# Kernel tuning notes

Measured on AMD Instinct MI355X. Metric: run time of the kernel, lower is better.

## Reference

```python
import jax, jax.numpy as jnp
import numpy as np


def _update_cv(features, labels, ave, cov, amount, class_num):
    # Segment-reduce formulation of the onehot-expand update_CV.
    N, A = features.shape
    C = class_num
    counts = jax.ops.segment_sum(jnp.ones((N,), features.dtype), labels, num_segments=C)  # [C]
    sums = jax.ops.segment_sum(features, labels, num_segments=C)  # [C, A]
    denom = jnp.where(counts == 0, 1.0, counts)[:, None]  # Amount_CxA with zeros -> 1
    ave_CxA = sums / denom
    # var_temp: sum over samples of (x - mean_label)^2, divided by count
    diff = features - ave_CxA[labels]  # [N, A]
    sq = jax.ops.segment_sum(diff * diff, labels, num_segments=C)
    var_temp = sq / denom
    sum_weight = counts[:, None]  # [C,1] broadcast over A
    weight_CV = sum_weight / (sum_weight + amount[:, None])
    weight_CV = jnp.nan_to_num(weight_CV, nan=0.0)
    additional_CV = weight_CV * (1 - weight_CV) * (ave - ave_CxA) ** 2
    new_cov = cov * (1 - weight_CV) + var_temp * weight_CV + additional_CV
    new_ave = ave * (1 - weight_CV) + ave_CxA * weight_CV
    new_amount = amount + counts
    return new_ave, new_cov, new_amount


def _isda_aug(fc_weight, y, labels, cv_matrix, ratio):
    # sigma2[n,c] = ratio * sum_a (W[c,a] - W[labels[n],a])^2 * CV[labels[n],a]
    # = ratio * ( (W^2) @ cv_n - 2 W @ (w_n * cv_n) + sum_a w_n^2 cv_n )
    cv_n = cv_matrix[labels]              # [N, A]
    w_n = fc_weight[labels]               # [N, A]
    t1 = cv_n @ (fc_weight ** 2).T        # [N, C]
    t2 = (w_n * cv_n) @ fc_weight.T       # [N, C]
    t3 = jnp.sum(w_n * w_n * cv_n, axis=1, keepdims=True)  # [N, 1]
    sigma2 = ratio * (t1 - 2.0 * t2 + t3)
    return y + 0.5 * sigma2


def setup_inputs() -> dict:
    key = jax.random.key(0)
    k1, k2, k3, k4 = jax.random.split(key, 4)
    N, A, C = 512, 2048, 1000
    features = jax.random.normal(k1, (N, A), dtype=jnp.float32)
    labels = jax.random.randint(k2, (N,), 0, C)
    fc_weight = jax.random.normal(k3, (C, A), dtype=jnp.float32) * 0.02
    fc_bias = jax.random.normal(k4, (C,), dtype=jnp.float32) * 0.02
    return {
        "features": features,
        "labels": labels,
        "fc_weight": fc_weight,
        "fc_bias": fc_bias,
        "ave_state": jnp.zeros((C, A), jnp.float32),
        "cov_state": jnp.zeros((C, A), jnp.float32),
        "amount_state": jnp.zeros((C,), jnp.float32),
        "ratio": 1,
    }


def reference(features, labels, fc_weight, fc_bias, ave_state, cov_state, amount_state, ratio):
    C = fc_weight.shape[0]
    # model head: y = features @ W^T + b (features come from backbone; detached for CV)
    y = features @ fc_weight.T + fc_bias
    new_ave, new_cov, new_amount = _update_cv(
        jax.lax.stop_gradient(features), labels, ave_state, cov_state, amount_state, C)
    isda_y = _isda_aug(fc_weight, y, labels, jax.lax.stop_gradient(new_cov), ratio)
    log_probs = jax.nn.log_softmax(isda_y, axis=1)
    loss = -jnp.mean(jnp.take_along_axis(log_probs, labels[:, None], axis=1))
    return loss, y, new_ave, new_cov, new_amount
```

## Files before the change

kernel.cpp:

```cpp
#include <hip/hip_runtime.h>
#include <hip/hip_bf16.h>

typedef short v8s __attribute__((ext_vector_type(8)));
typedef float v4f __attribute__((ext_vector_type(4)));

#define KSPLIT 4

static __device__ __forceinline__ float ldv(const void* p, size_t i, int f32m) {
    if (f32m) return ((const float*)p)[i];
    return __bfloat162float(((const __hip_bfloat16*)p)[i]);
}
static __device__ __forceinline__ void stv(void* p, size_t i, float v, int f32m) {
    if (f32m) ((float*)p)[i] = v;
    else ((__hip_bfloat16*)p)[i] = __float2bfloat16(v);
}
static __device__ __forceinline__ unsigned short f2bu(float x) {
    __hip_bfloat16 h = __float2bfloat16(x);
    return *(unsigned short*)&h;
}

static __device__ __forceinline__ float decode_scalar(const void* p) {
    unsigned u = *(const unsigned*)p;
    unsigned e32 = (u >> 23) & 0xff;
    if (e32 >= 97 && e32 <= 160) return __uint_as_float(u);
    unsigned lo = u & 0xffffu;
    unsigned e16 = (lo >> 7) & 0xff;
    if ((u >> 16) == 0 && e16 >= 97 && e16 <= 160)
        return __uint_as_float(lo << 16);
    return (float)(int)u;
}

static __device__ __forceinline__ int block_sniff(const void* feat) {
    const __hip_bfloat16* p = (const __hip_bfloat16*)feat;
    float v = __bfloat162float(p[threadIdx.x & 255]);
    int bad = !(fabsf(v) < 1e10f);
    return __syncthreads_or(bad) ? 1 : 0;
}

__device__ __forceinline__ float wave_sum(float v) {
    #pragma unroll
    for (int o = 32; o > 0; o >>= 1) v += __shfl_down(v, o, 64);
    return v;
}
__device__ __forceinline__ float wave_max(float v) {
    #pragma unroll
    for (int o = 32; o > 0; o >>= 1) v = fmaxf(v, __shfl_down(v, o, 64));
    return v;
}

static __device__ __forceinline__ void ld16(unsigned short* lds, const unsigned short* g) {
    __builtin_amdgcn_global_load_lds(
        (const __attribute__((address_space(1))) unsigned int*)g,
        (__attribute__((address_space(3))) unsigned int*)lds,
        16, 0, 0);
}

__global__ __launch_bounds__(256) void accum_stats(
        const void* __restrict__ feat, const int* __restrict__ labels,
        float* __restrict__ sums, float* __restrict__ sqs,
        float* __restrict__ counts, unsigned short* __restrict__ featb,
        int Nn, int A) {
    int f32m = block_sniff(feat);
    int idx = blockIdx.x * 256 + threadIdx.x;
    if (idx >= Nn * A) return;
    int n = idx / A;
    int a = idx - n * A;
    int l = labels[n];
    float x = ldv(feat, idx, f32m);
    featb[idx] = f2bu(x);
    atomicAdd(&sums[(size_t)l * A + a], x);
    atomicAdd(&sqs[(size_t)l * A + a], x * x);
    if (a == 0) atomicAdd(&counts[l], 1.0f);
}

__global__ __launch_bounds__(256) void finalize_stats(
        const float* __restrict__ sums, const float* __restrict__ sqs,
        const float* __restrict__ counts,
        const void* __restrict__ ave, const void* __restrict__ cov,
        const void* __restrict__ amount, const void* __restrict__ W,
        const void* __restrict__ feat,
        void* __restrict__ out, size_t off_ave, size_t off_cov, size_t off_amt,
        unsigned short* __restrict__ Wb, unsigned short* __restrict__ W2b,
        unsigned short* __restrict__ Cb, unsigned short* __restrict__ Gb,
        float* __restrict__ T3c,
        int C, int A) {
    __shared__ float sb[4];
    int f32m = block_sniff(feat);
    int idx = blockIdx.x * 256 + threadIdx.x;
    int c = idx / A;
    int a = idx - c * A;
    float cnt = counts[c];
    float denom = cnt > 0.f ? cnt : 1.f;
    float mean = sums[idx] / denom;
    float var = (sqs[idx] - cnt * mean * mean) / denom;
    var = fmaxf(var, 0.f);
    float amt = ldv(amount, c, f32m);
    float tot = cnt + amt;
    float w = tot > 0.f ? (cnt / tot) : 0.f;
    float av = ldv(ave, idx, f32m);
    float cv = ldv(cov, idx, f32m);
    float d = av - mean;
    float ncv = cv * (1.f - w) + var * w + w * (1.f - w) * d * d;
    float nav = av * (1.f - w) + mean * w;
    stv(out, off_cov + idx, ncv, f32m);
    stv(out, off_ave + idx, nav, f32m);
    float wv = ldv(W, idx, f32m);
    Wb[idx] = f2bu(wv);
    W2b[idx] = f2bu(wv * wv);
    Cb[idx] = f2bu(ncv);
    Gb[idx] = f2bu(ncv * wv);
    if (a == 0) stv(out, off_amt + c, amt + cnt, f32m);
    float s = wave_sum(wv * wv * ncv);
    int lane = threadIdx.x & 63, wid = threadIdx.x >> 6;
    if (lane == 0) sb[wid] = s;
    __syncthreads();
    if (threadIdx.x == 0) atomicAdd(&T3c[c], sb[0] + sb[1] + sb[2] + sb[3]);
}

__global__ __launch_bounds__(256) void triple_gemm_mfma(
        const unsigned short* __restrict__ featb,
        const unsigned short* __restrict__ Wb,
        const unsigned short* __restrict__ W2b,
        const unsigned short* __restrict__ Cb,
        const unsigned short* __restrict__ Gb,
        const int* __restrict__ labels,
        float* __restrict__ accY, float* __restrict__ accT1, float* __restrict__ accT2,
        int Cpad, int A) {
    __shared__ unsigned short sA[10240];
    __shared__ int sLab[64];
    int tid = threadIdx.x, wv = tid >> 6, lane = tid & 63;
    int n0 = blockIdx.y * 64, j0 = blockIdx.x * 64;
    int kslice = A / KSPLIT;
    int k0 = blockIdx.z * kslice;
    if (tid < 64) sLab[tid] = labels[n0 + tid];
    __syncthreads();

    int r = lane & 15, q = lane >> 4;
    int fr = wv * 16 + r;
    const unsigned short* pF = featb + (size_t)(n0 + fr) * A + k0 + q * 8;
    int lab = sLab[fr];
    const unsigned short* pC = Cb + (size_t)lab * A + k0 + q * 8;
    const unsigned short* pG = Gb + (size_t)lab * A + k0 + q * 8;
    const unsigned short* pW = Wb + (size_t)(j0 + fr) * A + k0 + q * 8;
    const unsigned short* pQ = W2b + (size_t)(j0 + fr) * A + k0 + q * 8;
    unsigned short* dF = &sA[0    + wv * 512];
    unsigned short* dC = &sA[2048 + wv * 512];
    unsigned short* dG = &sA[4096 + wv * 512];
    unsigned short* dW = &sA[6144 + wv * 512];
    unsigned short* dQ = &sA[8192 + wv * 512];

    v4f aY[4] = {{0,0,0,0},{0,0,0,0},{0,0,0,0},{0,0,0,0}};
    v4f aT1[4] = {{0,0,0,0},{0,0,0,0},{0,0,0,0},{0,0,0,0}};
    v4f aT2[4] = {{0,0,0,0},{0,0,0,0},{0,0,0,0},{0,0,0,0}};

    for (int kk = 0; kk < kslice; kk += 32) {
        ld16(dF, pF); ld16(dC, pC); ld16(dG, pG); ld16(dW, pW); ld16(dQ, pQ);
        pF += 32; pC += 32; pG += 32; pW += 32; pQ += 32;
        __syncthreads();
        v8s f = *(v8s*)&sA[0    + wv * 512 + lane * 8];
        v8s c = *(v8s*)&sA[2048 + wv * 512 + lane * 8];
        v8s g = *(v8s*)&sA[4096 + wv * 512 + lane * 8];
        #pragma unroll
        for (int t = 0; t < 4; ++t) {
            v8s w  = *(v8s*)&sA[6144 + t * 512 + lane * 8];
            v8s w2 = *(v8s*)&sA[8192 + t * 512 + lane * 8];
            aY[t]  = __builtin_amdgcn_mfma_f32_16x16x32_bf16(f, w,  aY[t],  0, 0, 0);
            aT1[t] = __builtin_amdgcn_mfma_f32_16x16x32_bf16(c, w2, aT1[t], 0, 0, 0);
            aT2[t] = __builtin_amdgcn_mfma_f32_16x16x32_bf16(g, w,  aT2[t], 0, 0, 0);
        }
        __syncthreads();
    }

    int quad = lane >> 4, colb = lane & 15;
    #pragma unroll
    for (int t = 0; t < 4; ++t) {
        int j = j0 + t * 16 + colb;
        #pragma unroll
        for (int rr = 0; rr < 4; ++rr) {
            int n = n0 + wv * 16 + quad * 4 + rr;
            size_t idx = (size_t)n * Cpad + j;
            atomicAdd(&accY[idx],  aY[t][rr]);
            atomicAdd(&accT1[idx], aT1[t][rr]);
            atomicAdd(&accT2[idx], aT2[t][rr]);
        }
    }
}

__global__ __launch_bounds__(256) void epilogue(
        const float* __restrict__ accY, const float* __restrict__ accT1,
        const float* __restrict__ accT2, const float* __restrict__ T3c,
        const void* __restrict__ bias, const void* __restrict__ feat,
        const int* __restrict__ labels,
        void* __restrict__ out, size_t off_y,
        float* __restrict__ isda, int C, int Cpad, const void* ratio_p) {
    int f32m = block_sniff(feat);
    int n = blockIdx.y;
    int j = blockIdx.x * 256 + threadIdx.x;
    if (j >= C) return;
    float ratio = decode_scalar(ratio_p);
    float t3 = T3c[labels[n]];
    size_t idx = (size_t)n * Cpad + j;
    float yv = accY[idx] + ldv(bias, j, f32m);
    stv(out, off_y + (size_t)n * C + j, yv, f32m);
    isda[idx] = yv + 0.5f * ratio * (accT1[idx] - 2.f * accT2[idx] + t3);
}

__global__ __launch_bounds__(256) void row_loss(
        const float* __restrict__ isda, const int* __restrict__ labels,
        float* __restrict__ rowloss, int C, int Cpad) {
    __shared__ float sb[4];
    __shared__ float bcast;
    int n = blockIdx.x;
    const float* row = isda + (size_t)n * Cpad;
    float m = -3.4e38f;
    for (int j = threadIdx.x; j < C; j += 256) m = fmaxf(m, row[j]);
    m = wave_max(m);
    int lane = threadIdx.x & 63, wid = threadIdx.x >> 6;
    if (lane == 0) sb[wid] = m;
    __syncthreads();
    if (threadIdx.x == 0)
        bcast = fmaxf(fmaxf(sb[0], sb[1]), fmaxf(sb[2], sb[3]));
    __syncthreads();
    m = bcast;
    __syncthreads();
    float s = 0.f;
    for (int j = threadIdx.x; j < C; j += 256) s += expf(row[j] - m);
    s = wave_sum(s);
    if (lane == 0) sb[wid] = s;
    __syncthreads();
    if (threadIdx.x == 0) {
        float tot = sb[0] + sb[1] + sb[2] + sb[3];
        rowloss[n] = m + logf(tot) - row[labels[n]];
    }
}

__global__ __launch_bounds__(256) void final_loss(
        const float* __restrict__ rowloss, void* __restrict__ out,
        const void* __restrict__ feat, int Nn) {
    __shared__ float sb[4];
    int f32m = block_sniff(feat);
    float s = 0.f;
    for (int i = threadIdx.x; i < Nn; i += 256) s += rowloss[i];
    s = wave_sum(s);
    int lane = threadIdx.x & 63, wid = threadIdx.x >> 6;
    if (lane == 0) sb[wid] = s;
    __syncthreads();
    if (threadIdx.x == 0)
        stv(out, 0, (sb[0] + sb[1] + sb[2] + sb[3]) / (float)Nn, f32m);
}

extern "C" void kernel_launch(void* const* d_in, const int* in_sizes, int n_in,
                              void* d_out, int out_size, void* d_ws, size_t ws_size,
                              hipStream_t stream) {
    const void* feat   = d_in[0];
    const int*  labels = (const int*)d_in[1];
    const void* W      = d_in[2];
    const void* bias   = d_in[3];
    const void* ave    = d_in[4];
    const void* cov    = d_in[5];
    const void* amount = d_in[6];
    const void* ratiop = d_in[7];

    int NA = in_sizes[0];
    int Nn = in_sizes[1];
    int C  = in_sizes[3];
    int A  = NA / Nn;
    int CA = in_sizes[2];
    int Cpad = ((C + 255) / 256) * 256;
    size_t NC = (size_t)Nn * Cpad;

    size_t off_y   = 1;
    size_t off_ave = off_y + (size_t)Nn * C;
    size_t off_cov = off_ave + (size_t)CA;
    size_t off_amt = off_cov + (size_t)CA;

    float* ws = (float*)d_ws;
    float* w_counts = ws;
    float* w_T3c    = ws + 1024;
    float* w_sums   = ws + 2048;
    float* w_sqs    = w_sums + CA;
    float* w_accY   = w_sqs + CA;
    float* w_accT1  = w_accY + NC;
    float* w_accT2  = w_accT1 + NC;
    float* w_isda   = w_accT2 + NC;
    float* w_rowls  = w_isda + NC;
    unsigned short* w_featb = (unsigned short*)(w_rowls + 1024);
    unsigned short* w_Wb    = w_featb + NA;
    unsigned short* w_W2b   = w_Wb + CA;
    unsigned short* w_Cb    = w_W2b + CA;
    unsigned short* w_Gb    = w_Cb + CA;

    hipMemsetAsync(ws, 0, (size_t)(2048 + 2 * (size_t)CA + 3 * NC) * sizeof(float), stream);

    accum_stats<<<(NA + 255) / 256, 256, 0, stream>>>(feat, labels, w_sums, w_sqs,
                                                      w_counts, w_featb, Nn, A);
    finalize_stats<<<(CA + 255) / 256, 256, 0, stream>>>(
        w_sums, w_sqs, w_counts, ave, cov, amount, W, feat,
        d_out, off_ave, off_cov, off_amt,
        w_Wb, w_W2b, w_Cb, w_Gb, w_T3c, C, A);
    dim3 g3(Cpad / 64, Nn / 64, KSPLIT);
    triple_gemm_mfma<<<g3, 256, 0, stream>>>(w_featb, w_Wb, w_W2b, w_Cb, w_Gb,
                                             labels, w_accY, w_accT1, w_accT2, Cpad, A);
    dim3 g4((C + 255) / 256, Nn);
    epilogue<<<g4, 256, 0, stream>>>(w_accY, w_accT1, w_accT2, w_T3c, bias, feat,
                                     labels, d_out, off_y, w_isda, C, Cpad, ratiop);
    row_loss<<<Nn, 256, 0, stream>>>(w_isda, labels, w_rowls, C, Cpad);
    final_loss<<<1, 256, 0, stream>>>(w_rowls, d_out, feat, Nn);
}
```

Baseline: 163.7 us.

## Replace atomic scatter stats with counting-sort gather and split-K partial buffers

Replaces the atomic per-element scatter of sums and squares with a counting sort of labels followed by a gather-based per-class reduction inside finalize_stats. The split-K GEMM now writes per-slice partial buffers instead of issuing atomics, and the epilogue and row loss are fused into one kernel that sums the partials. Together these remove the large workspace memset and most global atomics. In exchange, per-class statistics are now computed from bf16-rounded features, and the partial buffers add extra memory traffic.

Measured after the change: 142.3 us (median of 2 runs). 1.15x faster.

```diff
diff --git a/kernel.cpp b/kernel.cpp
--- a/kernel.cpp
+++ b/kernel.cpp
@@ -17,6 +17,9 @@
 static __device__ __forceinline__ unsigned short f2bu(float x) {
     __hip_bfloat16 h = __float2bfloat16(x);
     return *(unsigned short*)&h;
+}
+static __device__ __forceinline__ float bu2f(unsigned short u) {
+    return __uint_as_float(((unsigned)u) << 16);
 }
 
 static __device__ __forceinline__ float decode_scalar(const void* p) {
@@ -55,45 +58,80 @@
         16, 0, 0);
 }
 
-__global__ __launch_bounds__(256) void accum_stats(
-        const void* __restrict__ feat, const int* __restrict__ labels,
-        float* __restrict__ sums, float* __restrict__ sqs,
-        float* __restrict__ counts, unsigned short* __restrict__ featb,
-        int Nn, int A) {
+__global__ __launch_bounds__(1024) void count_sort(
+        const int* __restrict__ labels, int* __restrict__ counts,
+        int* __restrict__ offs, int* __restrict__ rows, int Nn, int C) {
+    __shared__ int h[1024];
+    __shared__ int o[1024];
+    __shared__ int cur[1024];
+    int tid = threadIdx.x;
+    h[tid] = 0;
+    __syncthreads();
+    for (int i = tid; i < Nn; i += 1024) atomicAdd(&h[labels[i]], 1);
+    __syncthreads();
+    o[tid] = h[tid];
+    __syncthreads();
+    for (int d = 1; d < 1024; d <<= 1) {
+        int v = (tid >= d) ? o[tid - d] : 0;
+        __syncthreads();
+        o[tid] += v;
+        __syncthreads();
+    }
+    int excl = o[tid] - h[tid];
+    counts[tid] = h[tid];
+    offs[tid] = excl;
+    cur[tid] = excl;
+    __syncthreads();
+    for (int i = tid; i < Nn; i += 1024) {
+        int pos = atomicAdd(&cur[labels[i]], 1);
+        rows[pos] = i;
+    }
+}
+
+__global__ __launch_bounds__(256) void prep(
+        const void* __restrict__ feat, unsigned short* __restrict__ featb, int total) {
     int f32m = block_sniff(feat);
-    int idx = blockIdx.x * 256 + threadIdx.x;
-    if (idx >= Nn * A) return;
-    int n = idx / A;
-    int a = idx - n * A;
-    int l = labels[n];
-    float x = ldv(feat, idx, f32m);
-    featb[idx] = f2bu(x);
-    atomicAdd(&sums[(size_t)l * A + a], x);
-    atomicAdd(&sqs[(size_t)l * A + a], x * x);
-    if (a == 0) atomicAdd(&counts[l], 1.0f);
+    int i = (blockIdx.x * 256 + threadIdx.x) * 8;
+    if (i >= total) return;
+    if (f32m) {
+        const float* f = (const float*)feat + i;
+        unsigned short r[8];
+        #pragma unroll
+        for (int u = 0; u < 8; ++u) r[u] = f2bu(f[u]);
+        *(v8s*)(featb + i) = *(v8s*)r;
+    } else {
+        *(v8s*)(featb + i) = *(const v8s*)((const unsigned short*)feat + i);
+    }
 }
 
 __global__ __launch_bounds__(256) void finalize_stats(
-        const float* __restrict__ sums, const float* __restrict__ sqs,
-        const float* __restrict__ counts,
+        const unsigned short* __restrict__ featb,
+        const int* __restrict__ counts, const int* __restrict__ offs,
+        const int* __restrict__ rows,
         const void* __restrict__ ave, const void* __restrict__ cov,
         const void* __restrict__ amount, const void* __restrict__ W,
         const void* __restrict__ feat,
         void* __restrict__ out, size_t off_ave, size_t off_cov, size_t off_amt,
         unsigned short* __restrict__ Wb, unsigned short* __restrict__ W2b,
         unsigned short* __restrict__ Cb, unsigned short* __restrict__ Gb,
-        float* __restrict__ T3c,
-        int C, int A) {
+        float* __restrict__ T3p, int A, int A8) {
     __shared__ float sb[4];
     int f32m = block_sniff(feat);
-    int idx = blockIdx.x * 256 + threadIdx.x;
-    int c = idx / A;
-    int a = idx - c * A;
-    float cnt = counts[c];
-    float denom = cnt > 0.f ? cnt : 1.f;
-    float mean = sums[idx] / denom;
-    float var = (sqs[idx] - cnt * mean * mean) / denom;
-    var = fmaxf(var, 0.f);
+    int c = blockIdx.y;
+    int a = blockIdx.x * 256 + threadIdx.x;
+    size_t idx = (size_t)c * A + a;
+    int cnti = counts[c];
+    int start = offs[c];
+    float s1 = 0.f, s2 = 0.f;
+    for (int i = 0; i < cnti; ++i) {
+        float x = bu2f(featb[(size_t)rows[start + i] * A + a]);
+        s1 += x;
+        s2 += x * x;
+    }
+    float cnt = (float)cnti;
+    float denom = cnti > 0 ? cnt : 1.f;
+    float mean = s1 / denom;
+    float var = fmaxf((s2 - cnt * mean * mean) / denom, 0.f);
     float amt = ldv(amount, c, f32m);
     float tot = cnt + amt;
     float w = tot > 0.f ? (cnt / tot) : 0.f;
@@ -114,7 +152,7 @@
     int lane = threadIdx.x & 63, wid = threadIdx.x >> 6;
     if (lane == 0) sb[wid] = s;
     __syncthreads();
-    if (threadIdx.x == 0) atomicAdd(&T3c[c], sb[0] + sb[1] + sb[2] + sb[3]);
+    if (threadIdx.x == 0) T3p[(size_t)c * A8 + blockIdx.x] = sb[0] + sb[1] + sb[2] + sb[3];
 }
 
 __global__ __launch_bounds__(256) void triple_gemm_mfma(
@@ -124,8 +162,8 @@
         const unsigned short* __restrict__ Cb,
         const unsigned short* __restrict__ Gb,
         const int* __restrict__ labels,
-        float* __restrict__ accY, float* __restrict__ accT1, float* __restrict__ accT2,
-        int Cpad, int A) {
+        float* __restrict__ partY, float* __restrict__ partT1, float* __restrict__ partT2,
+        int Cpad, int A, size_t NC) {
     __shared__ unsigned short sA[10240];
     __shared__ int sLab[64];
     int tid = threadIdx.x, wv = tid >> 6, lane = tid & 63;
@@ -171,6 +209,9 @@
         __syncthreads();
     }
 
+    float* pY = partY + (size_t)blockIdx.z * NC;
+    float* p1 = partT1 + (size_t)blockIdx.z * NC;
+    float* p2 = partT2 + (size_t)blockIdx.z * NC;
     int quad = lane >> 4, colb = lane & 15;
     #pragma unroll
     for (int t = 0; t < 4; ++t) {
@@ -179,59 +220,70 @@
         for (int rr = 0; rr < 4; ++rr) {
             int n = n0 + wv * 16 + quad * 4 + rr;
             size_t idx = (size_t)n * Cpad + j;
-            atomicAdd(&accY[idx],  aY[t][rr]);
-            atomicAdd(&accT1[idx], aT1[t][rr]);
-            atomicAdd(&accT2[idx], aT2[t][rr]);
+            pY[idx] = aY[t][rr];
+            p1[idx] = aT1[t][rr];
+            p2[idx] = aT2[t][rr];
         }
     }
 }
 
-__global__ __launch_bounds__(256) void epilogue(
-        const float* __restrict__ accY, const float* __restrict__ accT1,
-        const float* __restrict__ accT2, const float* __restrict__ T3c,
+__global__ __launch_bounds__(256) void epilogue_rowloss(
+        const float* __restrict__ partY, const float* __restrict__ partT1,
+        const float* __restrict__ partT2, const float* __restrict__ T3p,
         const void* __restrict__ bias, const void* __restrict__ feat,
         const int* __restrict__ labels,
         void* __restrict__ out, size_t off_y,
-        float* __restrict__ isda, int C, int Cpad, const void* ratio_p) {
+        float* __restrict__ rowloss,
+        int C, int Cpad, int A8, const void* ratio_p, size_t NC) {
+    __shared__ float sb[4];
+    __shared__ float sM;
+    __shared__ float sLabVal;
     int f32m = block_sniff(feat);
-    int n = blockIdx.y;
-    int j = blockIdx.x * 256 + threadIdx.x;
-    if (j >= C) return;
+    int tid = threadIdx.x;
+    int n = blockIdx.x;
+    int lab = labels[n];
+    float t3 = 0.f;
+    for (int i = 0; i < A8; ++i) t3 += T3p[(size_t)lab * A8 + i];
     float ratio = decode_scalar(ratio_p);
-    float t3 = T3c[labels[n]];
-    size_t idx = (size_t)n * Cpad + j;
-    float yv = accY[idx] + ldv(bias, j, f32m);
-    stv(out, off_y + (size_t)n * C + j, yv, f32m);
-    isda[idx] = yv + 0.5f * ratio * (accT1[idx] - 2.f * accT2[idx] + t3);
-}
-
-__global__ __launch_bounds__(256) void row_loss(
-        const float* __restrict__ isda, const int* __restrict__ labels,
-        float* __restrict__ rowloss, int C, int Cpad) {
-    __shared__ float sb[4];
-    __shared__ float bcast;
-    int n = blockIdx.x;
-    const float* row = isda + (size_t)n * Cpad;
+
+    float vals[8];
+    int nu = Cpad >> 8;
     float m = -3.4e38f;
-    for (int j = threadIdx.x; j < C; j += 256) m = fmaxf(m, row[j]);
+    for (int u = 0; u < nu; ++u) {
+        int j = u * 256 + tid;
+        float v = -3.4e38f;
+        if (j < C) {
+            size_t idx = (size_t)n * Cpad + j;
+            float y = 0.f, t1 = 0.f, t2 = 0.f;
+            #pragma unroll
+            for (int z = 0; z < KSPLIT; ++z) {
+                y  += partY[z * NC + idx];
+                t1 += partT1[z * NC + idx];
+                t2 += partT2[z * NC + idx];
+            }
+            y += ldv(bias, j, f32m);
+            stv(out, off_y + (size_t)n * C + j, y, f32m);
+            v = y + 0.5f * ratio * (t1 - 2.f * t2 + t3);
+            if (j == lab) sLabVal = v;
+        }
+        vals[u] = v;
+        m = fmaxf(m, v);
+    }
     m = wave_max(m);
-    int lane = threadIdx.x & 63, wid = threadIdx.x >> 6;
+    int lane = tid & 63, wid = tid >> 6;
     if (lane == 0) sb[wid] = m;
     __syncthreads();
-    if (threadIdx.x == 0)
-        bcast = fmaxf(fmaxf(sb[0], sb[1]), fmaxf(sb[2], sb[3]));
-    __syncthreads();
-    m = bcast;
-    __syncthreads();
+    if (tid == 0) sM = fmaxf(fmaxf(sb[0], sb[1]), fmaxf(sb[2], sb[3]));
+    __syncthreads();
+    m = sM;
     float s = 0.f;
-    for (int j = threadIdx.x; j < C; j += 256) s += expf(row[j] - m);
+    for (int u = 0; u < nu; ++u) s += expf(vals[u] - m);
+    __syncthreads();
     s = wave_sum(s);
     if (lane == 0) sb[wid] = s;
     __syncthreads();
-    if (threadIdx.x == 0) {
-        float tot = sb[0] + sb[1] + sb[2] + sb[3];
-        rowloss[n] = m + logf(tot) - row[labels[n]];
-    }
+    if (tid == 0)
+        rowloss[n] = m + logf(sb[0] + sb[1] + sb[2] + sb[3]) - sLabVal;
 }
 
 __global__ __launch_bounds__(256) void final_loss(
@@ -267,6 +319,7 @@
     int A  = NA / Nn;
     int CA = in_sizes[2];
     int Cpad = ((C + 255) / 256) * 256;
+    int A8 = A / 256;
     size_t NC = (size_t)Nn * Cpad;
 
     size_t off_y   = 1;
@@ -274,36 +327,34 @@
     size_t off_cov = off_ave + (size_t)CA;
     size_t off_amt = off_cov + (size_t)CA;
 
-    float* ws = (float*)d_ws;
-    float* w_counts = ws;
-    float* w_T3c    = ws + 1024;
-    float* w_sums   = ws + 2048;
-    float* w_sqs    = w_sums + CA;
-    float* w_accY   = w_sqs + CA;
-    float* w_accT1  = w_accY + NC;
-    float* w_accT2  = w_accT1 + NC;
-    float* w_isda   = w_accT2 + NC;
-    float* w_rowls  = w_isda + NC;
-    unsigned short* w_featb = (unsigned short*)(w_rowls + 1024);
+    char* ws = (char*)d_ws;
+    int*   w_cnt  = (int*)ws;
+    int*   w_off  = w_cnt + 1024;
+    int*   w_rows = w_off + 1024;
+    float* w_T3p  = (float*)(w_rows + 1024);
+    float* w_rowls = w_T3p + 8192;
+    float* w_partY  = w_rowls + 1024;
+    float* w_partT1 = w_partY + KSPLIT * NC;
+    float* w_partT2 = w_partT1 + KSPLIT * NC;
+    unsigned short* w_featb = (unsigned short*)(w_partT2 + KSPLIT * NC);
     unsigned short* w_Wb    = w_featb + NA;
     unsigned short* w_W2b   = w_Wb + CA;
     unsigned short* w_Cb    = w_W2b + CA;
     unsigned short* w_Gb    = w_Cb + CA;
 
-    hipMemsetAsync(ws, 0, (size_t)(2048 + 2 * (size_t)CA + 3 * NC) * sizeof(float), stream);
-
-    accum_stats<<<(NA + 255) / 256, 256, 0, stream>>>(feat, labels, w_sums, w_sqs,
-                                                      w_counts, w_featb, Nn, A);
-    finalize_stats<<<(CA + 255) / 256, 256, 0, stream>>>(
-        w_sums, w_sqs, w_counts, ave, cov, amount, W, feat,
-        d_out, off_ave, off_cov, off_amt,
-        w_Wb, w_W2b, w_Cb, w_Gb, w_T3c, C, A);
+    count_sort<<<1, 1024, 0, stream>>>(labels, w_cnt, w_off, w_rows, Nn, C);
+    prep<<<NA / 2048, 256, 0, stream>>>(feat, w_featb, NA);
+    dim3 g2(A8, C);
+    finalize_stats<<<g2, 256, 0, stream>>>(w_featb, w_cnt, w_off, w_rows,
+                                           ave, cov, amount, W, feat,
+                                           d_out, off_ave, off_cov, off_amt,
+                                           w_Wb, w_W2b, w_Cb, w_Gb, w_T3p, A, A8);
     dim3 g3(Cpad / 64, Nn / 64, KSPLIT);
     triple_gemm_mfma<<<g3, 256, 0, stream>>>(w_featb, w_Wb, w_W2b, w_Cb, w_Gb,
-                                             labels, w_accY, w_accT1, w_accT2, Cpad, A);
-    dim3 g4((C + 255) / 256, Nn);
-    epilogue<<<g4, 256, 0, stream>>>(w_accY, w_accT1, w_accT2, w_T3c, bias, feat,
-                                     labels, d_out, off_y, w_isda, C, Cpad, ratiop);
-    row_loss<<<Nn, 256, 0, stream>>>(w_isda, labels, w_rowls, C, Cpad);
+                                             labels, w_partY, w_partT1, w_partT2,
+                                             Cpad, A, NC);
+    epilogue_rowloss<<<Nn, 256, 0, stream>>>(w_partY, w_partT1, w_partT2, w_T3p,
+                                             bias, feat, labels, d_out, off_y,
+                                             w_rowls, C, Cpad, A8, ratiop, NC);
     final_loss<<<1, 256, 0, stream>>>(w_rowls, d_out, feat, Nn);
 }
```
